# Performance work log

Hardware: AMD Instinct MI355X
Metric: run time of the kernel (lower is better)

The kernel has to match this reference:

```python
import jax, jax.numpy as jnp
import numpy as np

N = 100000
E = 800000
HID = 512
HEADS = 8
F = HID // HEADS  # 64


def setup_inputs() -> dict:
    key = jax.random.key(0)
    k = jax.random.split(key, 8)
    in_nodes_features = jax.random.normal(k[0], (N, HID), dtype=jnp.float32)
    edge_index = jax.random.randint(k[1], (2, E), 0, N, dtype=jnp.int64)
    # xavier_normal gain=1.414 for W: std = gain * sqrt(2/(fan_in+fan_out))
    std_w = 1.414 * np.sqrt(2.0 / (HID + HID))
    W = jax.random.normal(k[2], (HID, HID), dtype=jnp.float32) * std_w
    b_lin = jnp.zeros((HID,), dtype=jnp.float32)
    std_s = 1.414 * np.sqrt(2.0 / (HEADS + F))  # xavier on (1,H,F) treats fan dims loosely; use per-slice
    a_src = jax.random.normal(k[3], (1, HEADS, F), dtype=jnp.float32) * std_s
    a_tgt = jax.random.normal(k[4], (1, HEADS, F), dtype=jnp.float32) * std_s
    bias = jnp.zeros((HID,), dtype=jnp.float32)
    prelu_a = jnp.asarray(0.25, dtype=jnp.float32)  # PReLU default init
    return {
        "in_nodes_features": in_nodes_features,
        "edge_index": edge_index,
        "W": W,
        "b_lin": b_lin,
        "a_src": a_src,
        "a_tgt": a_tgt,
        "bias": bias,
        "prelu_a": prelu_a,
    }


def reference(in_nodes_features, edge_index, W, b_lin, a_src, a_tgt, bias, prelu_a):
    num_nodes = in_nodes_features.shape[0]
    src, trg = edge_index[0], edge_index[1]

    # projection: [N, HID] -> [N, HEADS, F]
    proj = (in_nodes_features @ W.T + b_lin).reshape(num_nodes, HEADS, F)

    # per-node attention scores [N, HEADS]
    scores_source = jnp.sum(proj * a_src, axis=-1)
    scores_target = jnp.sum(proj * a_tgt, axis=-1)

    # lift to edges and score: [E, HEADS]
    scores_per_edge = jax.nn.leaky_relu(
        scores_source[src] + scores_target[trg], negative_slope=0.01
    )

    # neighborhood-aware softmax (global max subtraction as in original)
    exp_scores = jnp.exp(scores_per_edge - jnp.max(scores_per_edge))
    denom = jax.ops.segment_sum(exp_scores, trg, num_segments=num_nodes)  # [N, HEADS]
    attn = exp_scores / (denom[trg] + 1e-16)  # [E, HEADS]

    # weighted aggregation: [E, HEADS, F] scatter-add -> [N, HEADS, F]
    weighted = proj[src] * attn[:, :, None]
    out = jax.ops.segment_sum(weighted, trg, num_segments=num_nodes)
    out = out.reshape(num_nodes, HID) + bias

    # PReLU with single shared parameter
    return jnp.where(out >= 0, out, prelu_a * out)
```

## Files before the change

kernel.cpp:

```cpp
#include <hip/hip_runtime.h>
#include <stdint.h>

#define N_NODES 100000
#define N_EDGES 800000
#define HIDDIM 512
#define HEADS 8
#define FDIM 64

typedef __attribute__((ext_vector_type(4))) float f32x4;
typedef __attribute__((ext_vector_type(8))) short short8;
typedef __attribute__((ext_vector_type(8))) unsigned short ushort8;

static constexpr size_t OFF_PROJ   = 0;
static constexpr size_t OFF_SSRC   = 102400000;
static constexpr size_t OFF_STGT   = 105600000;
static constexpr size_t OFF_COUNTS = 108800000;
static constexpr size_t OFF_CURSOR = 109200000;
static constexpr size_t OFF_ROWOFF = 109600000;
static constexpr size_t OFF_BSUM   = 110000000;
static constexpr size_t OFF_BMAXS  = 110004096;
static constexpr size_t OFF_BMAXT  = 110006144;
static constexpr size_t OFF_M      = 110008192;
static constexpr size_t OFF_SSORT  = 110008208;
static constexpr size_t OFF_WB     = 113208208;
static constexpr size_t ZERO_BYTES = 800000;

__device__ __forceinline__ unsigned short f2bf(float f) {
  unsigned int u = __builtin_bit_cast(unsigned int, f);
  u += 0x7FFFu + ((u >> 16) & 1u);
  return (unsigned short)(u >> 16);
}
__device__ __forceinline__ float bf2f(unsigned short s) {
  unsigned int u = ((unsigned int)s) << 16;
  return __builtin_bit_cast(float, u);
}
__device__ __forceinline__ void gload_lds16(const void* g, void* l) {
  __builtin_amdgcn_global_load_lds((const __attribute__((address_space(1))) unsigned int*)g,
                                   (__attribute__((address_space(3))) unsigned int*)l, 16, 0, 0);
}

__global__ __launch_bounds__(256) void convert_w(const float* __restrict__ W,
                                                 unsigned short* __restrict__ Wb) {
  int i = blockIdx.x * 256 + threadIdx.x;
  const float4 v0 = *(const float4*)&W[(size_t)i * 8];
  const float4 v1 = *(const float4*)&W[(size_t)i * 8 + 4];
  ushort8 u;
  u[0] = f2bf(v0.x); u[1] = f2bf(v0.y); u[2] = f2bf(v0.z); u[3] = f2bf(v0.w);
  u[4] = f2bf(v1.x); u[5] = f2bf(v1.y); u[6] = f2bf(v1.z); u[7] = f2bf(v1.w);
  *(ushort8*)&Wb[(size_t)i * 8] = u;
}

__global__ __launch_bounds__(512) void gemm_proj(
    const float* __restrict__ X, const unsigned short* __restrict__ Wb,
    const float* __restrict__ b_lin, const float* __restrict__ a_src,
    const float* __restrict__ a_tgt,
    unsigned short* __restrict__ proj, float* __restrict__ s_src,
    float* __restrict__ s_tgt) {
  __shared__ __align__(16) unsigned short Al[128 * 64];
  __shared__ __align__(16) unsigned short Bl[256 * 64];
  const int t = threadIdx.x;
  const int bm = blockIdx.x, bn = blockIdx.y;
  const int lane = t & 63, wid = t >> 6;
  const int wr = wid >> 2, wc = wid & 3;

  f32x4 acc[4][4] = {};

  const int brow0 = bn * 256 + wid * 32 + (lane >> 3);
  const int bsrc_c = ((lane & 7) ^ (lane >> 3)) * 8;

  for (int kt = 0; kt < 8; ++kt) {
#pragma unroll
    for (int i = 0; i < 4; ++i)
      gload_lds16(&Wb[(size_t)(brow0 + i * 8) * 512 + kt * 64 + bsrc_c],
                  &Bl[(wid * 4 + i) * 512]);
#pragma unroll
    for (int i = 0; i < 2; ++i) {
      int idx8 = i * 512 + t;
      int row = idx8 >> 3, ck = idx8 & 7;
      int grow = bm * 128 + row;
      if (grow >= N_NODES) grow = N_NODES - 1;
      const float4 v0 = *(const float4*)&X[(size_t)grow * 512 + kt * 64 + ck * 8];
      const float4 v1 = *(const float4*)&X[(size_t)grow * 512 + kt * 64 + ck * 8 + 4];
      ushort8 u;
      u[0] = f2bf(v0.x); u[1] = f2bf(v0.y); u[2] = f2bf(v0.z); u[3] = f2bf(v0.w);
      u[4] = f2bf(v1.x); u[5] = f2bf(v1.y); u[6] = f2bf(v1.z); u[7] = f2bf(v1.w);
      *(ushort8*)&Al[row * 64 + ((ck ^ (row & 7)) * 8)] = u;
    }
    __syncthreads();
#pragma unroll
    for (int kk = 0; kk < 2; ++kk) {
      short8 af[4], bfr[4];
#pragma unroll
      for (int i = 0; i < 4; ++i) {
        int row = wr * 64 + i * 16 + (lane & 15);
        int ck = (kk * 4 + (lane >> 4)) ^ (row & 7);
        af[i] = *(const short8*)&Al[row * 64 + ck * 8];
      }
#pragma unroll
      for (int j = 0; j < 4; ++j) {
        int row = wc * 64 + j * 16 + (lane & 15);
        int ck = (kk * 4 + (lane >> 4)) ^ (row & 7);
        bfr[j] = *(const short8*)&Bl[row * 64 + ck * 8];
      }
#pragma unroll
      for (int i = 0; i < 4; ++i)
#pragma unroll
        for (int j = 0; j < 4; ++j)
          acc[i][j] = __builtin_amdgcn_mfma_f32_16x16x32_bf16(af[i], bfr[j], acc[i][j], 0, 0, 0);
    }
    __syncthreads();
  }

  const int col_head_base = bn * 256 + wc * 64;
  const int h = col_head_base >> 6;
  float asr[4], atg[4], bl[4];
#pragma unroll
  for (int j = 0; j < 4; ++j) {
    int f = j * 16 + (lane & 15);
    asr[j] = a_src[h * FDIM + f];
    atg[j] = a_tgt[h * FDIM + f];
    bl[j] = b_lin[col_head_base + f];
  }
#pragma unroll
  for (int i = 0; i < 4; ++i) {
#pragma unroll
    for (int r = 0; r < 4; ++r) {
      int grow = bm * 128 + wr * 64 + i * 16 + (lane >> 4) * 4 + r;
      float v[4];
      float ps = 0.f, pt = 0.f;
#pragma unroll
      for (int j = 0; j < 4; ++j) {
        v[j] = acc[i][j][r] + bl[j];
        ps += v[j] * asr[j];
        pt += v[j] * atg[j];
      }
#pragma unroll
      for (int m = 1; m < 16; m <<= 1) {
        ps += __shfl_xor(ps, m);
        pt += __shfl_xor(pt, m);
      }
      if (grow < N_NODES) {
#pragma unroll
        for (int j = 0; j < 4; ++j)
          proj[(size_t)grow * 512 + col_head_base + j * 16 + (lane & 15)] = f2bf(v[j]);
        if ((lane & 15) == 0) {
          s_src[grow * HEADS + h] = ps;
          s_tgt[grow * HEADS + h] = pt;
        }
      }
    }
  }
}

__global__ void maxred1(const float* __restrict__ s_src, const float* __restrict__ s_tgt,
                        float* __restrict__ bmax_s, float* __restrict__ bmax_t) {
  int t = threadIdx.x;
  float ms = -1e30f, mt = -1e30f;
  for (int i = blockIdx.x * 256 + t; i < N_NODES * HEADS; i += 512 * 256) {
    ms = fmaxf(ms, s_src[i]);
    mt = fmaxf(mt, s_tgt[i]);
  }
#pragma unroll
  for (int m = 1; m < 64; m <<= 1) {
    ms = fmaxf(ms, __shfl_xor(ms, m));
    mt = fmaxf(mt, __shfl_xor(mt, m));
  }
  __shared__ float shs[4], sht[4];
  if ((t & 63) == 0) { shs[t >> 6] = ms; sht[t >> 6] = mt; }
  __syncthreads();
  if (t == 0) {
    ms = fmaxf(fmaxf(shs[0], shs[1]), fmaxf(shs[2], shs[3]));
    mt = fmaxf(fmaxf(sht[0], sht[1]), fmaxf(sht[2], sht[3]));
    bmax_s[blockIdx.x] = ms;
    bmax_t[blockIdx.x] = mt;
  }
}
__global__ void maxred2(const float* __restrict__ bmax_s, const float* __restrict__ bmax_t,
                        float* __restrict__ M) {
  int t = threadIdx.x;
  float ms = bmax_s[t], mt = bmax_t[t];
#pragma unroll
  for (int m = 1; m < 64; m <<= 1) {
    ms = fmaxf(ms, __shfl_xor(ms, m));
    mt = fmaxf(mt, __shfl_xor(mt, m));
  }
  __shared__ float shs[8], sht[8];
  if ((t & 63) == 0) { shs[t >> 6] = ms; sht[t >> 6] = mt; }
  __syncthreads();
  if (t == 0) {
    for (int i = 1; i < 8; ++i) { ms = fmaxf(ms, shs[i]); mt = fmaxf(mt, sht[i]); }
    M[0] = fmaxf(0.0f, ms + mt);
  }
}

__global__ void edge_hist(const int* __restrict__ ei, int* __restrict__ counts) {
  int e = blockIdx.x * 256 + threadIdx.x;
  if (e >= N_EDGES) return;
  atomicAdd(&counts[ei[N_EDGES + e]], 1);
}

__global__ void scan1(const int* __restrict__ counts, int* __restrict__ row_off,
                      int* __restrict__ bsum) {
  __shared__ int sh[256];
  int t = threadIdx.x, i = blockIdx.x * 256 + t;
  int v = (i < N_NODES) ? counts[i] : 0;
  sh[t] = v;
  __syncthreads();
  for (int off = 1; off < 256; off <<= 1) {
    int x = (t >= off) ? sh[t - off] : 0;
    __syncthreads();
    sh[t] += x;
    __syncthreads();
  }
  if (i < N_NODES) row_off[i] = sh[t] - v;
  if (t == 255) bsum[blockIdx.x] = sh[255];
}
__global__ void scan2(int* __restrict__ bsum, int nb) {
  __shared__ int sh[512];
  int t = threadIdx.x;
  int v = (t < nb) ? bsum[t] : 0;
  sh[t] = v;
  __syncthreads();
  for (int off = 1; off < 512; off <<= 1) {
    int x = (t >= off) ? sh[t - off] : 0;
    __syncthreads();
    sh[t] += x;
    __syncthreads();
  }
  if (t < nb) bsum[t] = sh[t] - v;
}
__global__ void scan3(int* __restrict__ row_off, const int* __restrict__ bsum) {
  int i = blockIdx.x * 256 + threadIdx.x;
  if (i < N_NODES) row_off[i] += bsum[blockIdx.x];
}

__global__ void edge_pass2(const int* __restrict__ ei, const int* __restrict__ row_off,
                           int* __restrict__ cursor, int* __restrict__ sorted_src) {
  int e = blockIdx.x * 256 + threadIdx.x;
  if (e >= N_EDGES) return;
  int src = ei[e], trg = ei[N_EDGES + e];
  int pos = row_off[trg] + atomicAdd(&cursor[trg], 1);
  sorted_src[pos] = src;
}

__global__ __launch_bounds__(256) void aggregate(
    const int* __restrict__ row_off, const int* __restrict__ counts,
    const int* __restrict__ sorted_src, const float* __restrict__ s_src,
    const float* __restrict__ s_tgt, const float* __restrict__ Mp,
    const unsigned short* __restrict__ proj,
    const float* __restrict__ bias, const float* __restrict__ prelu_a,
    float* __restrict__ out) {
  const int node = blockIdx.x * 4 + (threadIdx.x >> 6);
  if (node >= N_NODES) return;
  const int lane = threadIdx.x & 63;
  const int h = lane >> 3;
  const int f8 = (lane & 7) * 8;
  const int start = row_off[node], deg = counts[node];
  const float st = s_tgt[node * HEADS + h];
  const float M = Mp[0];

  float acc[8] = {};
  float dsum = 0.f;
  for (int jb = 0; jb < deg; jb += 4) {
    const int nb = deg - jb;
    int s[4];
#pragma unroll
    for (int i = 0; i < 4; ++i) s[i] = sorted_src[start + jb + (i < nb ? i : 0)];
    float x[4];
#pragma unroll
    for (int i = 0; i < 4; ++i) x[i] = s_src[s[i] * HEADS + h];
    ushort8 p[4];
#pragma unroll
    for (int i = 0; i < 4; ++i)
      p[i] = *(const ushort8*)&proj[(size_t)s[i] * 512 + h * 64 + f8];
#pragma unroll
    for (int i = 0; i < 4; ++i) {
      if (i < nb) {
        float xx = x[i] + st;
        float l = xx > 0.f ? xx : 0.01f * xx;
        float e = __expf(l - M);
        dsum += e;
#pragma unroll
        for (int k = 0; k < 8; ++k) acc[k] += e * bf2f(p[i][k]);
      }
    }
  }
  const float inv = 1.0f / (dsum + 1e-16f);
  const float pa = prelu_a[0];
  const int c = h * 64 + f8;
  float o[8];
#pragma unroll
  for (int k = 0; k < 8; ++k) {
    float v = acc[k] * inv + bias[c + k];
    o[k] = v >= 0.f ? v : pa * v;
  }
  float4* op = (float4*)&out[(size_t)node * 512 + c];
  op[0] = make_float4(o[0], o[1], o[2], o[3]);
  op[1] = make_float4(o[4], o[5], o[6], o[7]);
}

extern "C" void kernel_launch(void* const* d_in, const int* in_sizes, int n_in,
                              void* d_out, int out_size, void* d_ws, size_t ws_size,
                              hipStream_t stream) {
  const float* X = (const float*)d_in[0];
  const int* ei = (const int*)d_in[1];
  const float* W = (const float*)d_in[2];
  const float* b_lin = (const float*)d_in[3];
  const float* a_src = (const float*)d_in[4];
  const float* a_tgt = (const float*)d_in[5];
  const float* bias = (const float*)d_in[6];
  const float* prelu_a = (const float*)d_in[7];

  char* ws = (char*)d_ws;
  unsigned short* proj = (unsigned short*)(ws + OFF_PROJ);
  float* s_src = (float*)(ws + OFF_SSRC);
  float* s_tgt = (float*)(ws + OFF_STGT);
  int* counts = (int*)(ws + OFF_COUNTS);
  int* cursor = (int*)(ws + OFF_CURSOR);
  int* row_off = (int*)(ws + OFF_ROWOFF);
  int* bsum = (int*)(ws + OFF_BSUM);
  float* bmax_s = (float*)(ws + OFF_BMAXS);
  float* bmax_t = (float*)(ws + OFF_BMAXT);
  float* Mp = (float*)(ws + OFF_M);
  int* sorted_src = (int*)(ws + OFF_SSORT);
  unsigned short* Wb = (unsigned short*)(ws + OFF_WB);

  hipMemsetAsync(ws + OFF_COUNTS, 0, ZERO_BYTES, stream);

  convert_w<<<128, 256, 0, stream>>>(W, Wb);
  gemm_proj<<<dim3(782, 2), 512, 0, stream>>>(X, Wb, b_lin, a_src, a_tgt, proj, s_src, s_tgt);
  maxred1<<<512, 256, 0, stream>>>(s_src, s_tgt, bmax_s, bmax_t);
  maxred2<<<1, 512, 0, stream>>>(bmax_s, bmax_t, Mp);
  edge_hist<<<3125, 256, 0, stream>>>(ei, counts);
  scan1<<<391, 256, 0, stream>>>(counts, row_off, bsum);
  scan2<<<1, 512, 0, stream>>>(bsum, 391);
  scan3<<<391, 256, 0, stream>>>(row_off, bsum);
  edge_pass2<<<3125, 256, 0, stream>>>(ei, row_off, cursor, sorted_src);
  aggregate<<<25000, 256, 0, stream>>>(row_off, counts, sorted_src, s_src, s_tgt, Mp,
                                       proj, bias, prelu_a, (float*)d_out);
}
```

Measured before the change: 388.9 us.

## Double-buffer projection GEMM and shrink block tile to 128x128

The projection GEMM now uses two LDS buffers for the A and B tiles. The next k-slice of W is staged asynchronously and X is prefetched into registers while MFMAs run on the current slice, which removes one barrier per iteration. The block shrinks to 256 threads with a 128x128 output tile and the grid doubles along N. Latency hiding and occupancy should improve, but the fp32 X rows are now read and converted to bf16 by twice as many blocks.

```diff
diff --git a/kernel.cpp b/kernel.cpp
--- a/kernel.cpp
+++ b/kernel.cpp
@@ -50,43 +50,68 @@
   *(ushort8*)&Wb[(size_t)i * 8] = u;
 }
 
-__global__ __launch_bounds__(512) void gemm_proj(
+__global__ __launch_bounds__(256) void gemm_proj(
     const float* __restrict__ X, const unsigned short* __restrict__ Wb,
     const float* __restrict__ b_lin, const float* __restrict__ a_src,
     const float* __restrict__ a_tgt,
     unsigned short* __restrict__ proj, float* __restrict__ s_src,
     float* __restrict__ s_tgt) {
-  __shared__ __align__(16) unsigned short Al[128 * 64];
-  __shared__ __align__(16) unsigned short Bl[256 * 64];
+  __shared__ __align__(16) unsigned short Al[2][128 * 64];
+  __shared__ __align__(16) unsigned short Bl[2][128 * 64];
   const int t = threadIdx.x;
   const int bm = blockIdx.x, bn = blockIdx.y;
   const int lane = t & 63, wid = t >> 6;
-  const int wr = wid >> 2, wc = wid & 3;
+  const int wr = wid >> 1, wc = wid & 1;
 
   f32x4 acc[4][4] = {};
-
-  const int brow0 = bn * 256 + wid * 32 + (lane >> 3);
+  float4 va[4][2];
+
+  const int brow0 = bn * 128 + wid * 32 + (lane >> 3);
   const int bsrc_c = ((lane & 7) ^ (lane >> 3)) * 8;
 
+#define STAGE_B(kt, buf)                                                        \
+  {                                                                             \
+    _Pragma("unroll") for (int i = 0; i < 4; ++i)                               \
+        gload_lds16(&Wb[(size_t)(brow0 + i * 8) * 512 + (kt) * 64 + bsrc_c],    \
+                    &Bl[buf][(wid * 4 + i) * 512]);                             \
+  }
+#define LOAD_A(kt)                                                              \
+  {                                                                             \
+    _Pragma("unroll") for (int i = 0; i < 4; ++i) {                             \
+      int idx8 = i * 256 + t;                                                   \
+      int row = idx8 >> 3, ck = idx8 & 7;                                       \
+      int grow = bm * 128 + row;                                                \
+      if (grow >= N_NODES) grow = N_NODES - 1;                                  \
+      const float* p = &X[(size_t)grow * 512 + (kt) * 64 + ck * 8];             \
+      va[i][0] = *(const float4*)p;                                             \
+      va[i][1] = *(const float4*)(p + 4);                                       \
+    }                                                                           \
+  }
+#define WRITE_A(buf)                                                            \
+  {                                                                             \
+    _Pragma("unroll") for (int i = 0; i < 4; ++i) {                             \
+      int idx8 = i * 256 + t;                                                   \
+      int row = idx8 >> 3, ck = idx8 & 7;                                       \
+      ushort8 u;                                                                \
+      u[0] = f2bf(va[i][0].x); u[1] = f2bf(va[i][0].y);                         \
+      u[2] = f2bf(va[i][0].z); u[3] = f2bf(va[i][0].w);                         \
+      u[4] = f2bf(va[i][1].x); u[5] = f2bf(va[i][1].y);                         \
+      u[6] = f2bf(va[i][1].z); u[7] = f2bf(va[i][1].w);                         \
+      *(ushort8*)&Al[buf][row * 64 + ((ck ^ (row & 7)) * 8)] = u;               \
+    }                                                                           \
+  }
+
+  STAGE_B(0, 0);
+  LOAD_A(0);
+  WRITE_A(0);
+  __syncthreads();
+
   for (int kt = 0; kt < 8; ++kt) {
-#pragma unroll
-    for (int i = 0; i < 4; ++i)
-      gload_lds16(&Wb[(size_t)(brow0 + i * 8) * 512 + kt * 64 + bsrc_c],
-                  &Bl[(wid * 4 + i) * 512]);
-#pragma unroll
-    for (int i = 0; i < 2; ++i) {
-      int idx8 = i * 512 + t;
-      int row = idx8 >> 3, ck = idx8 & 7;
-      int grow = bm * 128 + row;
-      if (grow >= N_NODES) grow = N_NODES - 1;
-      const float4 v0 = *(const float4*)&X[(size_t)grow * 512 + kt * 64 + ck * 8];
-      const float4 v1 = *(const float4*)&X[(size_t)grow * 512 + kt * 64 + ck * 8 + 4];
-      ushort8 u;
-      u[0] = f2bf(v0.x); u[1] = f2bf(v0.y); u[2] = f2bf(v0.z); u[3] = f2bf(v0.w);
-      u[4] = f2bf(v1.x); u[5] = f2bf(v1.y); u[6] = f2bf(v1.z); u[7] = f2bf(v1.w);
-      *(ushort8*)&Al[row * 64 + ((ck ^ (row & 7)) * 8)] = u;
+    const int cur = kt & 1, nxt = cur ^ 1;
+    if (kt < 7) {
+      STAGE_B(kt + 1, nxt);
+      LOAD_A(kt + 1);
     }
-    __syncthreads();
 #pragma unroll
     for (int kk = 0; kk < 2; ++kk) {
       short8 af[4], bfr[4];
@@ -94,13 +119,13 @@
       for (int i = 0; i < 4; ++i) {
         int row = wr * 64 + i * 16 + (lane & 15);
         int ck = (kk * 4 + (lane >> 4)) ^ (row & 7);
-        af[i] = *(const short8*)&Al[row * 64 + ck * 8];
+        af[i] = *(const short8*)&Al[cur][row * 64 + ck * 8];
       }
 #pragma unroll
       for (int j = 0; j < 4; ++j) {
         int row = wc * 64 + j * 16 + (lane & 15);
         int ck = (kk * 4 + (lane >> 4)) ^ (row & 7);
-        bfr[j] = *(const short8*)&Bl[row * 64 + ck * 8];
+        bfr[j] = *(const short8*)&Bl[cur][row * 64 + ck * 8];
       }
 #pragma unroll
       for (int i = 0; i < 4; ++i)
@@ -108,10 +133,11 @@
         for (int j = 0; j < 4; ++j)
           acc[i][j] = __builtin_amdgcn_mfma_f32_16x16x32_bf16(af[i], bfr[j], acc[i][j], 0, 0, 0);
     }
-    __syncthreads();
-  }
-
-  const int col_head_base = bn * 256 + wc * 64;
+    if (kt < 7) WRITE_A(nxt);
+    __syncthreads();
+  }
+
+  const int col_head_base = bn * 128 + wc * 64;
   const int h = col_head_base >> 6;
   float asr[4], atg[4], bl[4];
 #pragma unroll
@@ -150,6 +176,9 @@
       }
     }
   }
+#undef STAGE_B
+#undef LOAD_A
+#undef WRITE_A
 }
 
 __global__ void maxred1(const float* __restrict__ s_src, const float* __restrict__ s_tgt,
@@ -328,7 +357,7 @@
   hipMemsetAsync(ws + OFF_COUNTS, 0, ZERO_BYTES, stream);
 
   convert_w<<<128, 256, 0, stream>>>(W, Wb);
-  gemm_proj<<<dim3(782, 2), 512, 0, stream>>>(X, Wb, b_lin, a_src, a_tgt, proj, s_src, s_tgt);
+  gemm_proj<<<dim3(782, 4), 256, 0, stream>>>(X, Wb, b_lin, a_src, a_tgt, proj, s_src, s_tgt);
   maxred1<<<512, 256, 0, stream>>>(s_src, s_tgt, bmax_s, bmax_t);
   maxred2<<<1, 512, 0, stream>>>(bmax_s, bmax_t, Mp);
   edge_hist<<<3125, 256, 0, stream>>>(ei, counts);
```

New measurement: 434.1 us. +11.6%, slower.

## Fuse max reduction into GEMM epilogue and merge small prep kernels

Applied to the files above, without the earlier changes.

Removes the two max-reduction kernels by having each GEMM wave compute its local score maxima and fold them into a global key via atomicMax on order-preserving float keys. Merges the weight conversion and edge histogram into a single prep kernel, and drops scan3 by adding the block prefix sum at each use site in edge_pass2 and aggregate. This cuts launch count and a re-read of the score arrays, at the cost of atomics in the GEMM epilogue and an extra bsum lookup per node. Padded GEMM rows beyond N also feed the max, but their values are just the bias-based scores and the max is only used for stabilization.

```diff
diff --git a/kernel.cpp b/kernel.cpp
--- a/kernel.cpp
+++ b/kernel.cpp
@@ -16,14 +16,12 @@
 static constexpr size_t OFF_STGT   = 105600000;
 static constexpr size_t OFF_COUNTS = 108800000;
 static constexpr size_t OFF_CURSOR = 109200000;
-static constexpr size_t OFF_ROWOFF = 109600000;
-static constexpr size_t OFF_BSUM   = 110000000;
-static constexpr size_t OFF_BMAXS  = 110004096;
-static constexpr size_t OFF_BMAXT  = 110006144;
-static constexpr size_t OFF_M      = 110008192;
-static constexpr size_t OFF_SSORT  = 110008208;
-static constexpr size_t OFF_WB     = 113208208;
-static constexpr size_t ZERO_BYTES = 800000;
+static constexpr size_t OFF_KEYS   = 109600000;
+static constexpr size_t OFF_ROWOFF = 109600016;
+static constexpr size_t OFF_BSUM   = 110000016;
+static constexpr size_t OFF_SSORT  = 110004112;
+static constexpr size_t OFF_WB     = 113204112;
+static constexpr size_t ZERO_BYTES = 800016;
 
 __device__ __forceinline__ unsigned short f2bf(float f) {
   unsigned int u = __builtin_bit_cast(unsigned int, f);
@@ -34,20 +32,33 @@
   unsigned int u = ((unsigned int)s) << 16;
   return __builtin_bit_cast(float, u);
 }
+__device__ __forceinline__ unsigned int fkey(float x) {
+  unsigned int b = __builtin_bit_cast(unsigned int, x);
+  return (b & 0x80000000u) ? ~b : (b | 0x80000000u);
+}
+__device__ __forceinline__ float fdec(unsigned int k) {
+  unsigned int b = (k & 0x80000000u) ? (k & 0x7FFFFFFFu) : ~k;
+  return __builtin_bit_cast(float, b);
+}
 __device__ __forceinline__ void gload_lds16(const void* g, void* l) {
   __builtin_amdgcn_global_load_lds((const __attribute__((address_space(1))) unsigned int*)g,
                                    (__attribute__((address_space(3))) unsigned int*)l, 16, 0, 0);
 }
 
-__global__ __launch_bounds__(256) void convert_w(const float* __restrict__ W,
-                                                 unsigned short* __restrict__ Wb) {
+__global__ __launch_bounds__(256) void prep(const float* __restrict__ W,
+                                            unsigned short* __restrict__ Wb,
+                                            const int* __restrict__ ei,
+                                            int* __restrict__ counts) {
   int i = blockIdx.x * 256 + threadIdx.x;
-  const float4 v0 = *(const float4*)&W[(size_t)i * 8];
-  const float4 v1 = *(const float4*)&W[(size_t)i * 8 + 4];
-  ushort8 u;
-  u[0] = f2bf(v0.x); u[1] = f2bf(v0.y); u[2] = f2bf(v0.z); u[3] = f2bf(v0.w);
-  u[4] = f2bf(v1.x); u[5] = f2bf(v1.y); u[6] = f2bf(v1.z); u[7] = f2bf(v1.w);
-  *(ushort8*)&Wb[(size_t)i * 8] = u;
+  if (i < 32768) {
+    const float4 v0 = *(const float4*)&W[(size_t)i * 8];
+    const float4 v1 = *(const float4*)&W[(size_t)i * 8 + 4];
+    ushort8 u;
+    u[0] = f2bf(v0.x); u[1] = f2bf(v0.y); u[2] = f2bf(v0.z); u[3] = f2bf(v0.w);
+    u[4] = f2bf(v1.x); u[5] = f2bf(v1.y); u[6] = f2bf(v1.z); u[7] = f2bf(v1.w);
+    *(ushort8*)&Wb[(size_t)i * 8] = u;
+  }
+  if (i < N_EDGES) atomicAdd(&counts[ei[N_EDGES + i]], 1);
 }
 
 __global__ __launch_bounds__(512) void gemm_proj(
@@ -55,7 +66,7 @@
     const float* __restrict__ b_lin, const float* __restrict__ a_src,
     const float* __restrict__ a_tgt,
     unsigned short* __restrict__ proj, float* __restrict__ s_src,
-    float* __restrict__ s_tgt) {
+    float* __restrict__ s_tgt, unsigned int* __restrict__ keys) {
   __shared__ __align__(16) unsigned short Al[128 * 64];
   __shared__ __align__(16) unsigned short Bl[256 * 64];
   const int t = threadIdx.x;
@@ -121,6 +132,7 @@
     atg[j] = a_tgt[h * FDIM + f];
     bl[j] = b_lin[col_head_base + f];
   }
+  float wms = -1e30f, wmt = -1e30f;
 #pragma unroll
   for (int i = 0; i < 4; ++i) {
 #pragma unroll
@@ -139,6 +151,8 @@
         ps += __shfl_xor(ps, m);
         pt += __shfl_xor(pt, m);
       }
+      wms = fmaxf(wms, ps);
+      wmt = fmaxf(wmt, pt);
       if (grow < N_NODES) {
 #pragma unroll
         for (int j = 0; j < 4; ++j)
@@ -150,53 +164,15 @@
       }
     }
   }
-}
-
-__global__ void maxred1(const float* __restrict__ s_src, const float* __restrict__ s_tgt,
-                        float* __restrict__ bmax_s, float* __restrict__ bmax_t) {
-  int t = threadIdx.x;
-  float ms = -1e30f, mt = -1e30f;
-  for (int i = blockIdx.x * 256 + t; i < N_NODES * HEADS; i += 512 * 256) {
-    ms = fmaxf(ms, s_src[i]);
-    mt = fmaxf(mt, s_tgt[i]);
-  }
-#pragma unroll
-  for (int m = 1; m < 64; m <<= 1) {
-    ms = fmaxf(ms, __shfl_xor(ms, m));
-    mt = fmaxf(mt, __shfl_xor(mt, m));
-  }
-  __shared__ float shs[4], sht[4];
-  if ((t & 63) == 0) { shs[t >> 6] = ms; sht[t >> 6] = mt; }
-  __syncthreads();
-  if (t == 0) {
-    ms = fmaxf(fmaxf(shs[0], shs[1]), fmaxf(shs[2], shs[3]));
-    mt = fmaxf(fmaxf(sht[0], sht[1]), fmaxf(sht[2], sht[3]));
-    bmax_s[blockIdx.x] = ms;
-    bmax_t[blockIdx.x] = mt;
-  }
-}
-__global__ void maxred2(const float* __restrict__ bmax_s, const float* __restrict__ bmax_t,
-                        float* __restrict__ M) {
-  int t = threadIdx.x;
-  float ms = bmax_s[t], mt = bmax_t[t];
-#pragma unroll
-  for (int m = 1; m < 64; m <<= 1) {
-    ms = fmaxf(ms, __shfl_xor(ms, m));
-    mt = fmaxf(mt, __shfl_xor(mt, m));
-  }
-  __shared__ float shs[8], sht[8];
-  if ((t & 63) == 0) { shs[t >> 6] = ms; sht[t >> 6] = mt; }
-  __syncthreads();
-  if (t == 0) {
-    for (int i = 1; i < 8; ++i) { ms = fmaxf(ms, shs[i]); mt = fmaxf(mt, sht[i]); }
-    M[0] = fmaxf(0.0f, ms + mt);
-  }
-}
-
-__global__ void edge_hist(const int* __restrict__ ei, int* __restrict__ counts) {
-  int e = blockIdx.x * 256 + threadIdx.x;
-  if (e >= N_EDGES) return;
-  atomicAdd(&counts[ei[N_EDGES + e]], 1);
+#pragma unroll
+  for (int m = 16; m < 64; m <<= 1) {
+    wms = fmaxf(wms, __shfl_xor(wms, m));
+    wmt = fmaxf(wmt, __shfl_xor(wmt, m));
+  }
+  if (lane == 0) {
+    atomicMax(&keys[0], fkey(wms));
+    atomicMax(&keys[1], fkey(wmt));
+  }
 }
 
 __global__ void scan1(const int* __restrict__ counts, int* __restrict__ row_off,
@@ -229,25 +205,22 @@
   }
   if (t < nb) bsum[t] = sh[t] - v;
 }
-__global__ void scan3(int* __restrict__ row_off, const int* __restrict__ bsum) {
-  int i = blockIdx.x * 256 + threadIdx.x;
-  if (i < N_NODES) row_off[i] += bsum[blockIdx.x];
-}
 
 __global__ void edge_pass2(const int* __restrict__ ei, const int* __restrict__ row_off,
-                           int* __restrict__ cursor, int* __restrict__ sorted_src) {
+                           const int* __restrict__ bsum, int* __restrict__ cursor,
+                           int* __restrict__ sorted_src) {
   int e = blockIdx.x * 256 + threadIdx.x;
   if (e >= N_EDGES) return;
   int src = ei[e], trg = ei[N_EDGES + e];
-  int pos = row_off[trg] + atomicAdd(&cursor[trg], 1);
+  int pos = row_off[trg] + bsum[trg >> 8] + atomicAdd(&cursor[trg], 1);
   sorted_src[pos] = src;
 }
 
 __global__ __launch_bounds__(256) void aggregate(
-    const int* __restrict__ row_off, const int* __restrict__ counts,
-    const int* __restrict__ sorted_src, const float* __restrict__ s_src,
-    const float* __restrict__ s_tgt, const float* __restrict__ Mp,
-    const unsigned short* __restrict__ proj,
+    const int* __restrict__ row_off, const int* __restrict__ bsum,
+    const int* __restrict__ counts, const int* __restrict__ sorted_src,
+    const float* __restrict__ s_src, const float* __restrict__ s_tgt,
+    const unsigned int* __restrict__ keys, const unsigned short* __restrict__ proj,
     const float* __restrict__ bias, const float* __restrict__ prelu_a,
     float* __restrict__ out) {
   const int node = blockIdx.x * 4 + (threadIdx.x >> 6);
@@ -255,9 +228,10 @@
   const int lane = threadIdx.x & 63;
   const int h = lane >> 3;
   const int f8 = (lane & 7) * 8;
-  const int start = row_off[node], deg = counts[node];
+  const int start = row_off[node] + bsum[node >> 8];
+  const int deg = counts[node];
   const float st = s_tgt[node * HEADS + h];
-  const float M = Mp[0];
+  const float M = fmaxf(0.0f, fdec(keys[0]) + fdec(keys[1]));
 
   float acc[8] = {};
   float dsum = 0.f;
@@ -317,25 +291,20 @@
   float* s_tgt = (float*)(ws + OFF_STGT);
   int* counts = (int*)(ws + OFF_COUNTS);
   int* cursor = (int*)(ws + OFF_CURSOR);
+  unsigned int* keys = (unsigned int*)(ws + OFF_KEYS);
   int* row_off = (int*)(ws + OFF_ROWOFF);
   int* bsum = (int*)(ws + OFF_BSUM);
-  float* bmax_s = (float*)(ws + OFF_BMAXS);
-  float* bmax_t = (float*)(ws + OFF_BMAXT);
-  float* Mp = (float*)(ws + OFF_M);
   int* sorted_src = (int*)(ws + OFF_SSORT);
   unsigned short* Wb = (unsigned short*)(ws + OFF_WB);
 
   hipMemsetAsync(ws + OFF_COUNTS, 0, ZERO_BYTES, stream);
 
-  convert_w<<<128, 256, 0, stream>>>(W, Wb);
-  gemm_proj<<<dim3(782, 2), 512, 0, stream>>>(X, Wb, b_lin, a_src, a_tgt, proj, s_src, s_tgt);
-  maxred1<<<512, 256, 0, stream>>>(s_src, s_tgt, bmax_s, bmax_t);
-  maxred2<<<1, 512, 0, stream>>>(bmax_s, bmax_t, Mp);
-  edge_hist<<<3125, 256, 0, stream>>>(ei, counts);
+  prep<<<3125, 256, 0, stream>>>(W, Wb, ei, counts);
+  gemm_proj<<<dim3(782, 2), 512, 0, stream>>>(X, Wb, b_lin, a_src, a_tgt, proj, s_src, s_tgt,
+                                              keys);
   scan1<<<391, 256, 0, stream>>>(counts, row_off, bsum);
   scan2<<<1, 512, 0, stream>>>(bsum, 391);
-  scan3<<<391, 256, 0, stream>>>(row_off, bsum);
-  edge_pass2<<<3125, 256, 0, stream>>>(ei, row_off, cursor, sorted_src);
-  aggregate<<<25000, 256, 0, stream>>>(row_off, counts, sorted_src, s_src, s_tgt, Mp,
+  edge_pass2<<<3125, 256, 0, stream>>>(ei, row_off, bsum, cursor, sorted_src);
+  aggregate<<<25000, 256, 0, stream>>>(row_off, bsum, counts, sorted_src, s_src, s_tgt, keys,
                                        proj, bias, prelu_a, (float*)d_out);
 }
```

After: 586.5 us. 50.8% more time.
